# Kernel optimization log

Measured on AMD Instinct MI355X. Metric: run time of the kernel, lower is better.

The kernel has to match this reference:

```python
import jax, jax.numpy as jnp
import numpy as np

S, B = 64, 256
CH_IN, CH_OUT, AUX, HID = 128, 128, 3, 32
EPS = 1e-5


def _ln(h, g, b):
    mu = jnp.mean(h, axis=-1, keepdims=True)
    var = jnp.mean(jnp.square(h - mu), axis=-1, keepdims=True)
    return (h - mu) * jax.lax.rsqrt(var + EPS) * g + b


def _hyper_mlp(z, W1, b1, g1, be1, W2, b2, g2, be2, W3, b3):
    # Linear -> LN -> ReLU -> Linear -> LN -> ReLU -> Linear (droprate=0)
    h = jax.nn.relu(_ln(jnp.einsum('sba,ha->sbh', z, W1) + b1, g1, be1))
    h = jax.nn.relu(_ln(jnp.einsum('sbh,kh->sbk', h, W2) + b2, g2, be2))
    return jnp.einsum('sbh,oh->sbo', h, W3) + b3


def setup_inputs() -> dict:
    key = jax.random.key(0)
    ks = jax.random.split(key, 24)
    f = lambda k, shp: (jax.random.normal(k, shp, dtype=jnp.float32) * 0.05)
    inp = {
        'x': jax.random.normal(ks[0], (S, B, CH_IN), dtype=jnp.float32),
        'z': jax.random.normal(ks[1], (S, B, AUX), dtype=jnp.float32),
        # weight-branch hypernet params
        'wW1': f(ks[2], (HID, AUX)), 'wb1': jnp.zeros((HID,), jnp.float32),
        'wg1': jnp.ones((HID,), jnp.float32), 'wbe1': jnp.zeros((HID,), jnp.float32),
        'wW2': f(ks[3], (HID, HID)), 'wb2': jnp.zeros((HID,), jnp.float32),
        'wg2': jnp.ones((HID,), jnp.float32), 'wbe2': jnp.zeros((HID,), jnp.float32),
        'wW3': f(ks[4], (CH_OUT * CH_IN, HID)), 'wb3': jnp.zeros((CH_OUT * CH_IN,), jnp.float32),
        # bias-branch hypernet params
        'bW1': f(ks[5], (HID, AUX)), 'bb1': jnp.zeros((HID,), jnp.float32),
        'bg1': jnp.ones((HID,), jnp.float32), 'bbe1': jnp.zeros((HID,), jnp.float32),
        'bW2': f(ks[6], (HID, HID)), 'bb2': jnp.zeros((HID,), jnp.float32),
        'bg2': jnp.ones((HID,), jnp.float32), 'bbe2': jnp.zeros((HID,), jnp.float32),
        'bW3': f(ks[7], (CH_OUT, HID)), 'bb3': jnp.zeros((CH_OUT,), jnp.float32),
    }
    return inp


def reference(x, z,
              wW1, wb1, wg1, wbe1, wW2, wb2, wg2, wbe2, wW3, wb3,
              bW1, bb1, bg1, bbe1, bW2, bb2, bg2, bbe2, bW3, bb3):
    # per-token weight: [S,B,ch_out*ch_in] -> [S,B,ch_out,ch_in]
    weight = _hyper_mlp(z, wW1, wb1, wg1, wbe1, wW2, wb2, wg2, wbe2, wW3, wb3)
    weight = weight.reshape(S, B, CH_OUT, CH_IN)
    bias = _hyper_mlp(z, bW1, bb1, bg1, bbe1, bW2, bb2, bg2, bbe2, bW3, bb3)
    # batched mat-vec: out[s,b,o] = sum_i weight[s,b,o,i] * x[s,b,i] + bias
    out = jnp.einsum('sboi,sbi->sbo', weight, x) + bias
    return out
```

## Files before the change

kernel.cpp:

```cpp
#include <hip/hip_runtime.h>
#include <hip/hip_bf16.h>
#include <stdint.h>

#define T_DIM   16384
#define KR      4288
#define NT      67
#define LN_EPS  1e-5f

typedef __attribute__((ext_vector_type(8))) short  short8;
typedef __attribute__((ext_vector_type(4))) float  f32x4;
typedef __attribute__((ext_vector_type(8))) __bf16 bf8;

__device__ __forceinline__ void g2l16(const ushort* g, ushort* l) {
  __builtin_amdgcn_global_load_lds(
      (const __attribute__((address_space(1))) uint32_t*)g,
      (__attribute__((address_space(3))) uint32_t*)l, 16, 0, 0);
}

__global__ __launch_bounds__(128) void prep_w3(
    const float* __restrict__ wW3, const float* __restrict__ wb3,
    const float* __restrict__ bW3, ushort* __restrict__ w3b)
{
  const int k = blockIdx.x * 128 + threadIdx.x;
  const int o = blockIdx.y;
  if (k >= KR) return;
  const int swz   = (o >> 1) & 3;
  const int slice = k >> 5;
  const int pc    = ((((k >> 3) & 3) ^ swz) << 3) | (k & 7);
  float v;
  if      (slice < 128) v = wW3[(o * 128 + slice) * 32 + pc];
  else if (slice < 132) v = wb3[o * 128 + (slice - 128) * 32 + pc];
  else if (slice == 132) v = bW3[o * 32 + pc];
  else                  v = 0.f;
  __bf16 b = (__bf16)v;
  w3b[(size_t)o * KR + k] = *(ushort*)&b;
}

__global__ __launch_bounds__(256) void fused_kernel(
    const float* __restrict__ x, const float* __restrict__ z,
    const float* __restrict__ wW1, const float* __restrict__ wb1,
    const float* __restrict__ wg1, const float* __restrict__ wbe1,
    const float* __restrict__ wW2, const float* __restrict__ wb2,
    const float* __restrict__ wg2, const float* __restrict__ wbe2,
    const float* __restrict__ bW1, const float* __restrict__ bb1,
    const float* __restrict__ bg1, const float* __restrict__ bbe1,
    const float* __restrict__ bW2, const float* __restrict__ bb2,
    const float* __restrict__ bg2, const float* __restrict__ bbe2,
    const float* __restrict__ bb3,
    const ushort* __restrict__ w3b, float* __restrict__ out)
{
  __shared__ __align__(16) ushort xs[64][136];
  __shared__ __align__(16) ushort bsm[3 * 8192];
  __shared__ float h2s[2][64][33];

  const int tid  = threadIdx.x;
  const int lane = tid & 63;
  const int wid  = tid >> 6;
  const int wr   = wid >> 1, wc = wid & 1;
  const int lm   = lane & 15, hc = lane >> 4, hbase = hc * 8;
  const int t0   = blockIdx.x * 64;

  auto stageB = [&](int buf, int ks2) {
#pragma unroll
    for (int it = 0; it < 4; ++it) {
      int idx = it * 256 + tid;
      int c = idx & 3, o = (idx >> 2) & 127, i2 = idx >> 9;
      const ushort* src = w3b + (size_t)o * KR + (ks2 * 2 + i2) * 32 + c * 8;
      g2l16(src, &bsm[buf * 8192 + idx * 8]);
    }
  };

  float bb3v[4];
#pragma unroll
  for (int n = 0; n < 4; ++n) bb3v[n] = bb3[wc * 64 + n * 16 + lm];

  stageB(0, 0);
  stageB(1, 1);

  {
    const int r = tid >> 2, q = tid & 3;
    const float* src = x + (size_t)(t0 + r) * 128 + q * 32;
#pragma unroll
    for (int u = 0; u < 8; ++u) {
      float4 v = *(const float4*)(src + u * 4);
      __bf16 c0 = (__bf16)v.x, c1 = (__bf16)v.y, c2 = (__bf16)v.z, c3 = (__bf16)v.w;
      ushort4 w;
      w.x = *(ushort*)&c0; w.y = *(ushort*)&c1; w.z = *(ushort*)&c2; w.w = *(ushort*)&c3;
      *(ushort4*)&xs[r][q * 32 + u * 4] = w;
    }
  }

  if (tid < 128) {
    const int br  = tid >> 6;
    const int row = tid & 63;
    const int tok = t0 + row;
    const float* W1  = br ? bW1  : wW1;  const float* b1  = br ? bb1  : wb1;
    const float* g1  = br ? bg1  : wg1;  const float* be1 = br ? bbe1 : wbe1;
    const float* W2  = br ? bW2  : wW2;  const float* b2  = br ? bb2  : wb2;
    const float* g2  = br ? bg2  : wg2;  const float* be2 = br ? bbe2 : wbe2;

    const float z0 = z[tok * 3 + 0], z1 = z[tok * 3 + 1], z2 = z[tok * 3 + 2];

    float h1[32];
    float s = 0.f, s2 = 0.f;
#pragma unroll
    for (int j = 0; j < 32; ++j) {
      float v = W1[j * 3] * z0 + W1[j * 3 + 1] * z1 + W1[j * 3 + 2] * z2 + b1[j];
      h1[j] = v; s += v; s2 += v * v;
    }
    float mu  = s * (1.f / 32.f);
    float var = fmaxf(s2 * (1.f / 32.f) - mu * mu, 0.f);
    float rr  = rsqrtf(var + LN_EPS);
#pragma unroll
    for (int j = 0; j < 32; ++j)
      h1[j] = fmaxf((h1[j] - mu) * rr * g1[j] + be1[j], 0.f);

    float h2a[32];
    s = 0.f; s2 = 0.f;
#pragma unroll
    for (int j = 0; j < 32; ++j) {
      float acc = b2[j];
#pragma unroll
      for (int kk = 0; kk < 8; ++kk) {
        float4 w = *(const float4*)&W2[j * 32 + kk * 4];
        acc += w.x * h1[kk * 4] + w.y * h1[kk * 4 + 1]
             + w.z * h1[kk * 4 + 2] + w.w * h1[kk * 4 + 3];
      }
      h2a[j] = acc; s += acc; s2 += acc * acc;
    }
    mu  = s * (1.f / 32.f);
    var = fmaxf(s2 * (1.f / 32.f) - mu * mu, 0.f);
    rr  = rsqrtf(var + LN_EPS);
#pragma unroll
    for (int j = 0; j < 32; ++j)
      h2s[br][row][j] = fmaxf((h2a[j] - mu) * rr * g2[j] + be2[j], 0.f);
  }

  __syncthreads();

  int rl[2];
  rl[0] = wr * 32 + lm;
  rl[1] = wr * 32 + 16 + lm;

  float h2f[2][8];
  short8 h2bf[2];
#pragma unroll
  for (int m = 0; m < 2; ++m) {
#pragma unroll
    for (int jj = 0; jj < 8; ++jj) h2f[m][jj] = h2s[0][rl[m]][hbase + jj];
    bf8 t;
#pragma unroll
    for (int jj = 0; jj < 8; ++jj) t[jj] = (__bf16)h2s[1][rl[m]][hbase + jj];
    h2bf[m] = *(short8*)&t;
  }

  int boffs[4][2];
#pragma unroll
  for (int n = 0; n < 4; ++n) {
    int o   = wc * 64 + n * 16 + lm;
    int swz = (o >> 1) & 3;
#pragma unroll
    for (int i2 = 0; i2 < 2; ++i2)
      boffs[n][i2] = ((i2 * 128 + o) * 4 + (hc ^ swz)) * 8;
  }

  f32x4 acc[2][4];
#pragma unroll
  for (int m = 0; m < 2; ++m)
#pragma unroll
    for (int n = 0; n < 4; ++n) acc[m][n] = (f32x4){0.f, 0.f, 0.f, 0.f};

  int cur = 0;
#pragma unroll 1
  for (int ks = 0; ks < NT; ++ks) {
    if (ks < NT - 1) asm volatile("s_waitcnt vmcnt(4)" ::: "memory");
    else             asm volatile("s_waitcnt vmcnt(0)" ::: "memory");
    __builtin_amdgcn_s_barrier();
    asm volatile("" ::: "memory");

    if (ks + 2 < NT) {
      int sb = cur + 2; if (sb >= 3) sb -= 3;
      stageB(sb, ks + 2);
    }

    short8 af[2][2];
    if (ks < 64) {
#pragma unroll
      for (int m = 0; m < 2; ++m) {
        uint32_t xp = *(const uint32_t*)&xs[rl[m]][2 * ks];
        union { uint32_t u; float f; } lo, hi;
        lo.u = xp << 16;
        hi.u = xp & 0xffff0000u;
        bf8 a0, a1;
#pragma unroll
        for (int jj = 0; jj < 8; ++jj) {
          a0[jj] = (__bf16)(lo.f * h2f[m][jj]);
          a1[jj] = (__bf16)(hi.f * h2f[m][jj]);
        }
        af[0][m] = *(short8*)&a0;
        af[1][m] = *(short8*)&a1;
      }
    } else if (ks < 66) {
#pragma unroll
      for (int i2 = 0; i2 < 2; ++i2) {
        int s = (ks - 64) * 2 + i2;
#pragma unroll
        for (int m = 0; m < 2; ++m)
          af[i2][m] = *(const short8*)&xs[rl[m]][s * 32 + hbase];
      }
    } else {
#pragma unroll
      for (int m = 0; m < 2; ++m) { af[0][m] = h2bf[m]; af[1][m] = h2bf[m]; }
    }

#pragma unroll
    for (int i2 = 0; i2 < 2; ++i2) {
#pragma unroll
      for (int n = 0; n < 4; ++n) {
        short8 bfr = *(const short8*)&bsm[cur * 8192 + boffs[n][i2]];
#pragma unroll
        for (int m = 0; m < 2; ++m)
          acc[m][n] = __builtin_amdgcn_mfma_f32_16x16x32_bf16(
              af[i2][m], bfr, acc[m][n], 0, 0, 0);
      }
    }

    cur = (cur == 2) ? 0 : cur + 1;
  }

#pragma unroll
  for (int m = 0; m < 2; ++m) {
    const int gr0 = t0 + wr * 32 + m * 16 + hc * 4;
#pragma unroll
    for (int n = 0; n < 4; ++n) {
      const int gc = wc * 64 + n * 16 + lm;
#pragma unroll
      for (int r_ = 0; r_ < 4; ++r_) {
        const int row = gr0 + r_;
        out[(size_t)row * 128 + gc] = acc[m][n][r_] + bb3v[n];
      }
    }
  }
}

extern "C" void kernel_launch(void* const* d_in, const int* in_sizes, int n_in,
                              void* d_out, int out_size, void* d_ws, size_t ws_size,
                              hipStream_t stream)
{
  const float* x    = (const float*)d_in[0];
  const float* z    = (const float*)d_in[1];
  const float* wW1  = (const float*)d_in[2];
  const float* wb1  = (const float*)d_in[3];
  const float* wg1  = (const float*)d_in[4];
  const float* wbe1 = (const float*)d_in[5];
  const float* wW2  = (const float*)d_in[6];
  const float* wb2  = (const float*)d_in[7];
  const float* wg2  = (const float*)d_in[8];
  const float* wbe2 = (const float*)d_in[9];
  const float* wW3  = (const float*)d_in[10];
  const float* wb3  = (const float*)d_in[11];
  const float* bW1  = (const float*)d_in[12];
  const float* bb1  = (const float*)d_in[13];
  const float* bg1  = (const float*)d_in[14];
  const float* bbe1 = (const float*)d_in[15];
  const float* bW2  = (const float*)d_in[16];
  const float* bb2  = (const float*)d_in[17];
  const float* bg2  = (const float*)d_in[18];
  const float* bbe2 = (const float*)d_in[19];
  const float* bW3  = (const float*)d_in[20];
  const float* bb3  = (const float*)d_in[21];

  ushort* w3b = (ushort*)d_ws;
  float*  outf = (float*)d_out;

  hipLaunchKernelGGL(prep_w3, dim3((KR + 127) / 128, 128), dim3(128), 0, stream,
                     wW3, wb3, bW3, w3b);
  hipLaunchKernelGGL(fused_kernel, dim3(256), dim3(256), 0, stream,
                     x, z,
                     wW1, wb1, wg1, wbe1, wW2, wb2, wg2, wbe2,
                     bW1, bb1, bg1, bbe1, bW2, bb2, bg2, bbe2,
                     bb3, w3b, outf);
}
```

Measured before the change: 66.63 us.

## Split output columns across two blocks and vectorize weight prep

The fused kernel now launches 512 blocks, each computing 64 tokens by 64 output channels instead of all 128, so the MI355X's many CUs get more blocks and each block stages half the B tile per step. The staging addresses become incrementing pointers, and h2 values are stored once as fp32 or bf16 with vector LDS writes. prep_w3 now converts eight elements per thread with float4 loads and 16-byte stores. In exchange, the hypernet MLP and the A-operand construction run twice per token group, once in each block of the pair.

```diff
diff --git a/kernel.cpp b/kernel.cpp
--- a/kernel.cpp
+++ b/kernel.cpp
@@ -17,23 +17,38 @@
       (__attribute__((address_space(3))) uint32_t*)l, 16, 0, 0);
 }
 
-__global__ __launch_bounds__(128) void prep_w3(
+__global__ __launch_bounds__(256) void prep_w3(
     const float* __restrict__ wW3, const float* __restrict__ wb3,
     const float* __restrict__ bW3, ushort* __restrict__ w3b)
 {
-  const int k = blockIdx.x * 128 + threadIdx.x;
-  const int o = blockIdx.y;
-  if (k >= KR) return;
-  const int swz   = (o >> 1) & 3;
-  const int slice = k >> 5;
-  const int pc    = ((((k >> 3) & 3) ^ swz) << 3) | (k & 7);
-  float v;
-  if      (slice < 128) v = wW3[(o * 128 + slice) * 32 + pc];
-  else if (slice < 132) v = wb3[o * 128 + (slice - 128) * 32 + pc];
-  else if (slice == 132) v = bW3[o * 32 + pc];
-  else                  v = 0.f;
-  __bf16 b = (__bf16)v;
-  w3b[(size_t)o * KR + k] = *(ushort*)&b;
+  const int cid = blockIdx.x * 256 + threadIdx.x;
+  const int o   = blockIdx.y;
+  if (cid >= KR / 8) return;
+  const int k0    = cid * 8;
+  const int slice = k0 >> 5;
+  const int q     = (k0 >> 3) & 3;
+  const int pcc   = q ^ ((o >> 1) & 3);
+  float v[8];
+  if (slice < 132) {
+    const float* src = (slice < 128)
+        ? wW3 + ((size_t)o * 128 + slice) * 32 + pcc * 8
+        : wb3 + (size_t)o * 128 + (slice - 128) * 32 + pcc * 8;
+    float4 a = *(const float4*)src;
+    float4 b = *(const float4*)(src + 4);
+    v[0]=a.x; v[1]=a.y; v[2]=a.z; v[3]=a.w; v[4]=b.x; v[5]=b.y; v[6]=b.z; v[7]=b.w;
+  } else if (slice == 132) {
+    const float* src = bW3 + (size_t)o * 32 + pcc * 8;
+    float4 a = *(const float4*)src;
+    float4 b = *(const float4*)(src + 4);
+    v[0]=a.x; v[1]=a.y; v[2]=a.z; v[3]=a.w; v[4]=b.x; v[5]=b.y; v[6]=b.z; v[7]=b.w;
+  } else {
+#pragma unroll
+    for (int j = 0; j < 8; ++j) v[j] = 0.f;
+  }
+  bf8 pk;
+#pragma unroll
+  for (int j = 0; j < 8; ++j) pk[j] = (__bf16)v[j];
+  *(short8*)(w3b + (size_t)o * KR + k0) = *(short8*)&pk;
 }
 
 __global__ __launch_bounds__(256) void fused_kernel(
@@ -50,32 +65,35 @@
     const ushort* __restrict__ w3b, float* __restrict__ out)
 {
   __shared__ __align__(16) ushort xs[64][136];
-  __shared__ __align__(16) ushort bsm[3 * 8192];
-  __shared__ float h2s[2][64][33];
+  __shared__ __align__(16) ushort bsm[3][4096];
+  __shared__ __align__(16) float  h2w_s[64][36];
+  __shared__ __align__(16) ushort h2b_s[64][40];
 
   const int tid  = threadIdx.x;
   const int lane = tid & 63;
   const int wid  = tid >> 6;
   const int wr   = wid >> 1, wc = wid & 1;
   const int lm   = lane & 15, hc = lane >> 4, hbase = hc * 8;
-  const int t0   = blockIdx.x * 64;
-
-  auto stageB = [&](int buf, int ks2) {
-#pragma unroll
-    for (int it = 0; it < 4; ++it) {
-      int idx = it * 256 + tid;
-      int c = idx & 3, o = (idx >> 2) & 127, i2 = idx >> 9;
-      const ushort* src = w3b + (size_t)o * KR + (ks2 * 2 + i2) * 32 + c * 8;
-      g2l16(src, &bsm[buf * 8192 + idx * 8]);
-    }
+  const int t0   = (blockIdx.x >> 1) * 64;
+  const int o0   = (blockIdx.x & 1) * 64;
+
+  const int idx0 = tid, idx1 = tid + 256;
+  const ushort* sp0 = w3b + (size_t)(o0 + ((idx0 >> 2) & 63)) * KR
+                          + (idx0 >> 8) * 32 + (idx0 & 3) * 8;
+  const ushort* sp1 = w3b + (size_t)(o0 + ((idx1 >> 2) & 63)) * KR
+                          + (idx1 >> 8) * 32 + (idx1 & 3) * 8;
+  auto stage = [&](int buf) {
+    g2l16(sp0, &bsm[buf][idx0 * 8]);
+    g2l16(sp1, &bsm[buf][idx1 * 8]);
+    sp0 += 64; sp1 += 64;
   };
 
-  float bb3v[4];
-#pragma unroll
-  for (int n = 0; n < 4; ++n) bb3v[n] = bb3[wc * 64 + n * 16 + lm];
-
-  stageB(0, 0);
-  stageB(1, 1);
+  stage(0);
+  stage(1);
+
+  float bb3v[2];
+#pragma unroll
+  for (int n = 0; n < 2; ++n) bb3v[n] = bb3[o0 + wc * 32 + n * 16 + lm];
 
   {
     const int r = tid >> 2, q = tid & 3;
@@ -131,9 +149,26 @@
     mu  = s * (1.f / 32.f);
     var = fmaxf(s2 * (1.f / 32.f) - mu * mu, 0.f);
     rr  = rsqrtf(var + LN_EPS);
-#pragma unroll
-    for (int j = 0; j < 32; ++j)
-      h2s[br][row][j] = fmaxf((h2a[j] - mu) * rr * g2[j] + be2[j], 0.f);
+    if (br == 0) {
+#pragma unroll
+      for (int j4 = 0; j4 < 8; ++j4) {
+        float4 w;
+        w.x = fmaxf((h2a[j4*4+0] - mu) * rr * g2[j4*4+0] + be2[j4*4+0], 0.f);
+        w.y = fmaxf((h2a[j4*4+1] - mu) * rr * g2[j4*4+1] + be2[j4*4+1], 0.f);
+        w.z = fmaxf((h2a[j4*4+2] - mu) * rr * g2[j4*4+2] + be2[j4*4+2], 0.f);
+        w.w = fmaxf((h2a[j4*4+3] - mu) * rr * g2[j4*4+3] + be2[j4*4+3], 0.f);
+        *(float4*)&h2w_s[row][j4 * 4] = w;
+      }
+    } else {
+#pragma unroll
+      for (int j8 = 0; j8 < 4; ++j8) {
+        bf8 pk;
+#pragma unroll
+        for (int j = 0; j < 8; ++j)
+          pk[j] = (__bf16)fmaxf((h2a[j8*8+j] - mu) * rr * g2[j8*8+j] + be2[j8*8+j], 0.f);
+        *(short8*)&h2b_s[row][j8 * 8] = *(short8*)&pk;
+      }
+    }
   }
 
   __syncthreads();
@@ -146,41 +181,40 @@
   short8 h2bf[2];
 #pragma unroll
   for (int m = 0; m < 2; ++m) {
-#pragma unroll
-    for (int jj = 0; jj < 8; ++jj) h2f[m][jj] = h2s[0][rl[m]][hbase + jj];
-    bf8 t;
-#pragma unroll
-    for (int jj = 0; jj < 8; ++jj) t[jj] = (__bf16)h2s[1][rl[m]][hbase + jj];
-    h2bf[m] = *(short8*)&t;
-  }
-
-  int boffs[4][2];
-#pragma unroll
-  for (int n = 0; n < 4; ++n) {
-    int o   = wc * 64 + n * 16 + lm;
-    int swz = (o >> 1) & 3;
+    float4 a = *(const float4*)&h2w_s[rl[m]][hbase];
+    float4 c = *(const float4*)&h2w_s[rl[m]][hbase + 4];
+    h2f[m][0]=a.x; h2f[m][1]=a.y; h2f[m][2]=a.z; h2f[m][3]=a.w;
+    h2f[m][4]=c.x; h2f[m][5]=c.y; h2f[m][6]=c.z; h2f[m][7]=c.w;
+    h2bf[m] = *(const short8*)&h2b_s[rl[m]][hbase];
+  }
+
+  int boffs[2][2];
+#pragma unroll
+  for (int n = 0; n < 2; ++n) {
+    int ol  = wc * 32 + n * 16 + lm;
+    int chc = hc ^ ((ol >> 1) & 3);
 #pragma unroll
     for (int i2 = 0; i2 < 2; ++i2)
-      boffs[n][i2] = ((i2 * 128 + o) * 4 + (hc ^ swz)) * 8;
-  }
-
-  f32x4 acc[2][4];
+      boffs[i2][n] = i2 * 2048 + ol * 32 + chc * 8;
+  }
+
+  f32x4 acc[2][2];
 #pragma unroll
   for (int m = 0; m < 2; ++m)
 #pragma unroll
-    for (int n = 0; n < 4; ++n) acc[m][n] = (f32x4){0.f, 0.f, 0.f, 0.f};
+    for (int n = 0; n < 2; ++n) acc[m][n] = (f32x4){0.f, 0.f, 0.f, 0.f};
 
   int cur = 0;
 #pragma unroll 1
   for (int ks = 0; ks < NT; ++ks) {
-    if (ks < NT - 1) asm volatile("s_waitcnt vmcnt(4)" ::: "memory");
+    if (ks < NT - 1) asm volatile("s_waitcnt vmcnt(2)" ::: "memory");
     else             asm volatile("s_waitcnt vmcnt(0)" ::: "memory");
     __builtin_amdgcn_s_barrier();
     asm volatile("" ::: "memory");
 
     if (ks + 2 < NT) {
       int sb = cur + 2; if (sb >= 3) sb -= 3;
-      stageB(sb, ks + 2);
+      stage(sb);
     }
 
     short8 af[2][2];
@@ -216,8 +250,8 @@
 #pragma unroll
     for (int i2 = 0; i2 < 2; ++i2) {
 #pragma unroll
-      for (int n = 0; n < 4; ++n) {
-        short8 bfr = *(const short8*)&bsm[cur * 8192 + boffs[n][i2]];
+      for (int n = 0; n < 2; ++n) {
+        short8 bfr = *(const short8*)&bsm[cur][boffs[i2][n]];
 #pragma unroll
         for (int m = 0; m < 2; ++m)
           acc[m][n] = __builtin_amdgcn_mfma_f32_16x16x32_bf16(
@@ -232,8 +266,8 @@
   for (int m = 0; m < 2; ++m) {
     const int gr0 = t0 + wr * 32 + m * 16 + hc * 4;
 #pragma unroll
-    for (int n = 0; n < 4; ++n) {
-      const int gc = wc * 64 + n * 16 + lm;
+    for (int n = 0; n < 2; ++n) {
+      const int gc = o0 + wc * 32 + n * 16 + lm;
 #pragma unroll
       for (int r_ = 0; r_ < 4; ++r_) {
         const int row = gr0 + r_;
@@ -273,9 +307,9 @@
   ushort* w3b = (ushort*)d_ws;
   float*  outf = (float*)d_out;
 
-  hipLaunchKernelGGL(prep_w3, dim3((KR + 127) / 128, 128), dim3(128), 0, stream,
+  hipLaunchKernelGGL(prep_w3, dim3(3, 128), dim3(256), 0, stream,
                      wW3, wb3, bW3, w3b);
-  hipLaunchKernelGGL(fused_kernel, dim3(256), dim3(256), 0, stream,
+  hipLaunchKernelGGL(fused_kernel, dim3(512), dim3(256), 0, stream,
                      x, z,
                      wW1, wb1, wg1, wbe1, wW2, wb2, wg2, wbe2,
                      bW1, bb1, bg1, bbe1, bW2, bb2, bg2, bbe2,
```

New measurement: 60.44 us. 1.1x faster.
